# Kernel optimization log

Measured on AMD Instinct MI355X. Metric: run time of the kernel, lower is better.

## Reference

```python
import jax, jax.numpy as jnp
import numpy as np

B, T, C = 4, 2048, 2048
H = 16
DK = C // H // 2          # head_k_dim = 64
DV = C // H               # head_v_dim = 128
KEY_DIM = H * DK          # 1024
VAL_DIM = H * DV          # 2048
CONV = 4                  # short conv kernel size
SCALE = DK ** -0.5


def setup_inputs() -> dict:
    key = jax.random.key(0)
    ks = jax.random.split(key, 12)
    s = 0.02
    rn = lambda k, shape, sc: (jax.random.normal(k, shape) * sc).astype(jnp.float32)
    return dict(
        x=jax.random.normal(ks[0], (B, T, C), jnp.float32),
        qk_w=rn(ks[1], (2 * KEY_DIM, C), s),
        vg_w=rn(ks[2], (2 * VAL_DIM, C), s),
        o_w=rn(ks[3], (C, VAL_DIM), s),
        a_w=rn(ks[4], (H, C), s),
        b_w=rn(ks[5], (H, C), s),
        b_bias=jnp.zeros((H,), jnp.float32),
        beta_bias=jnp.linspace(-1.5, 1.5, H).astype(jnp.float32),
        A_log=jnp.log(jax.random.uniform(ks[6], (H,), minval=2.0, maxval=8.0)).astype(jnp.float32),
        dt_bias=rn(ks[7], (H,), 0.1),
        q_conv_w=rn(ks[8], (KEY_DIM, 1, CONV), 0.3),
        k_conv_w=rn(ks[9], (KEY_DIM, 1, CONV), 0.3),
        v_conv_w=rn(ks[10], (VAL_DIM, 1, CONV), 0.3),
    )


def _causal_dwconv_silu(x, w):
    # x: [B,T,Ch], w: [Ch,1,K]; Conv1d(groups=Ch, padding=K-1) truncated to T == causal conv
    y = jax.lax.conv_general_dilated(
        jnp.transpose(x, (0, 2, 1)), w, (1,), [(w.shape[-1] - 1, 0)],
        dimension_numbers=('NCH', 'OIH', 'NCH'), feature_group_count=x.shape[-1])
    return jax.nn.silu(jnp.transpose(y, (0, 2, 1)))


def _l2norm(x, eps=1e-6):
    return x * jax.lax.rsqrt(jnp.sum(x * x, axis=-1, keepdims=True) + eps)


def _gated_delta_rule(q, k, v, g, beta):
    # q,k: [B,T,H,DK], v: [B,T,H,DV], g,beta: [B,T,H]
    q = _l2norm(q) * SCALE
    k = _l2norm(k)
    # time-major for scan
    qt, kt, vt = (jnp.moveaxis(a, 1, 0) for a in (q, k, v))
    gt, bt = jnp.moveaxis(g, 1, 0), jnp.moveaxis(beta, 1, 0)

    def step(S, inp):
        q_t, k_t, v_t, g_t, b_t = inp          # S: [B,H,DK,DV]
        S = S * jnp.exp(g_t)[..., None, None]  # forget gate
        mem = jnp.einsum('bhk,bhkv->bhv', k_t, S)
        delta = (v_t - mem) * b_t[..., None]   # beta-scaled delta update
        S = S + jnp.einsum('bhk,bhv->bhkv', k_t, delta)
        o_t = jnp.einsum('bhk,bhkv->bhv', q_t, S)
        return S, o_t

    S0 = jnp.zeros((q.shape[0], H, DK, DV), q.dtype)
    _, o = jax.lax.scan(step, S0, (qt, kt, vt, gt, bt))
    return jnp.moveaxis(o, 0, 1)  # [B,T,H,DV]


def reference(x, qk_w, vg_w, o_w, a_w, b_w, b_bias, beta_bias, A_log, dt_bias,
              q_conv_w, k_conv_w, v_conv_w):
    qk = x @ qk_w.T
    vg = x @ vg_w.T
    q, k = qk[..., :KEY_DIM], qk[..., KEY_DIM:]
    v, g_out = vg[..., :VAL_DIM], vg[..., VAL_DIM:]

    q = _causal_dwconv_silu(q, q_conv_w)
    k = _causal_dwconv_silu(k, k_conv_w)
    v = _causal_dwconv_silu(v, v_conv_w)

    Bm, Tm = x.shape[0], x.shape[1]
    q = q.reshape(Bm, Tm, H, DK)
    k = k.reshape(Bm, Tm, H, DK)
    v = v.reshape(Bm, Tm, H, DV)

    beta = jax.nn.sigmoid(x @ b_w.T + b_bias + beta_bias) * 2.0          # [B,T,H]
    g = -jnp.exp(A_log) * jax.nn.softplus(x @ a_w.T + dt_bias)           # [B,T,H]

    o = _gated_delta_rule(q, k, v, g, beta)                              # [B,T,H,DV]

    eps = jnp.finfo(o.dtype).eps
    o = o * jax.lax.rsqrt(jnp.mean(o * o, axis=-1, keepdims=True) + eps)  # rms_norm (no weight)
    o = o * jax.nn.silu(g_out.reshape(Bm, Tm, H, DV))
    return o.reshape(Bm, Tm, VAL_DIM) @ o_w.T
```

## Files before the change

kernel.cpp:

```cpp
#include <hip/hip_runtime.h>
#include <hip/hip_bf16.h>
#include <stdint.h>

#define B_ 4
#define T_ 2048
#define C_ 2048
#define H_ 16
#define DK_ 64
#define DV_ 128
#define BT_ (B_ * T_)

typedef __attribute__((ext_vector_type(8))) __bf16 bf16x8;
typedef __attribute__((ext_vector_type(4))) float f32x4;

__device__ __forceinline__ unsigned short f2bf(float f) {
    union { float f; uint32_t u; } v; v.f = f;
    uint32_t u = v.u;
    uint32_t r = u + 0x7FFFu + ((u >> 16) & 1u);
    return (unsigned short)(r >> 16);
}
__device__ __forceinline__ float bf2f(unsigned short h) {
    union { uint32_t u; float f; } v; v.u = ((uint32_t)h) << 16; return v.f;
}
__device__ __forceinline__ float siluf(float x) { return x / (1.f + expf(-x)); }

__device__ __forceinline__ float dpp_xor1_add(float x) {
    int t = __builtin_amdgcn_update_dpp(0, __float_as_int(x), 0xB1, 0xF, 0xF, true);
    return x + __int_as_float(t);
}
__device__ __forceinline__ float dpp_xor2_add(float x) {
    int t = __builtin_amdgcn_update_dpp(0, __float_as_int(x), 0x4E, 0xF, 0xF, true);
    return x + __int_as_float(t);
}

__device__ __forceinline__ void split_hl(float x, unsigned short& h, unsigned short& l) {
    unsigned short hu = f2bf(x);
    float lo = x - bf2f(hu);
    h = hu;
    l = (unsigned short)(__float_as_uint(lo) >> 16);
}

__global__ void cast_split_k(const float* __restrict__ in,
                             unsigned short* __restrict__ oh, unsigned short* __restrict__ ol, int n4) {
    int i = blockIdx.x * blockDim.x + threadIdx.x;
    if (i >= n4) return;
    float4 v = ((const float4*)in)[i];
    ushort4 h, l;
    split_hl(v.x, h.x, l.x); split_hl(v.y, h.y, l.y);
    split_hl(v.z, h.z, l.z); split_hl(v.w, h.w, l.w);
    ((ushort4*)oh)[i] = h;
    ((ushort4*)ol)[i] = l;
}

__global__ void cast_plain_k(const float* __restrict__ in, unsigned short* __restrict__ out, int n4) {
    int i = blockIdx.x * blockDim.x + threadIdx.x;
    if (i >= n4) return;
    float4 v = ((const float4*)in)[i];
    ushort4 o;
    o.x = f2bf(v.x); o.y = f2bf(v.y); o.z = f2bf(v.z); o.w = f2bf(v.w);
    ((ushort4*)out)[i] = o;
}

__global__ __launch_bounds__(256)
void cast_all_k(const float* __restrict__ x, const float* __restrict__ qk_w,
                const float* __restrict__ vg_w, const float* __restrict__ o_w,
                unsigned short* __restrict__ xh, unsigned short* __restrict__ xl,
                unsigned short* __restrict__ qkw_h, unsigned short* __restrict__ qkw_l,
                unsigned short* __restrict__ vgw_h, unsigned short* __restrict__ vgw_l,
                unsigned short* __restrict__ ow_bf) {
    const int NX = BT_ * C_ / 4;
    const int NW = 2048 * 2048 / 4;
    int i = blockIdx.x * blockDim.x + threadIdx.x;
    const float* src; unsigned short *dh, *dl; int j; bool split;
    if (i < NX)               { j = i;            src = x;                          dh = xh;    dl = xl;    split = true; }
    else if (i < NX + NW)     { j = i - NX;       src = qk_w;                       dh = qkw_h; dl = qkw_l; split = true; }
    else if (i < NX + 2 * NW) { j = i - NX - NW;  src = vg_w;                       dh = vgw_h; dl = vgw_l; split = true; }
    else if (i < NX + 3 * NW) { j = i - NX - 2*NW; src = vg_w + (size_t)2048*2048;  dh = vgw_h + (size_t)2048*2048; dl = nullptr; split = false; }
    else                      { j = i - NX - 3*NW; src = o_w;                       dh = ow_bf; dl = nullptr; split = false; }
    float4 v = ((const float4*)src)[j];
    ushort4 h, l;
    if (split) {
        split_hl(v.x, h.x, l.x); split_hl(v.y, h.y, l.y);
        split_hl(v.z, h.z, l.z); split_hl(v.w, h.w, l.w);
        ((ushort4*)dh)[j] = h;
        ((ushort4*)dl)[j] = l;
    } else {
        h.x = f2bf(v.x); h.y = f2bf(v.y); h.z = f2bf(v.z); h.w = f2bf(v.w);
        ((ushort4*)dh)[j] = h;
    }
}

__device__ __forceinline__ void gld_lds16(const unsigned short* gptr,
                                          unsigned short* lds_base) {
    __builtin_amdgcn_global_load_lds(
        (const __attribute__((address_space(1))) uint32_t*)(uintptr_t)gptr,
        (__attribute__((address_space(3))) uint32_t*)(uint32_t)(uintptr_t)lds_base,
        16, 0, 0);
}

template<bool DO_LO, bool F32OUT>
__global__ __launch_bounds__(256)
void gemm_bf(const unsigned short* __restrict__ Ah, const unsigned short* __restrict__ Al, int lda,
             const unsigned short* __restrict__ Wh, const unsigned short* __restrict__ Wl,
             void* __restrict__ Cout, int M, int N, int K) {
    __shared__ __align__(16) unsigned short sAh[128 * 64];
    __shared__ __align__(16) unsigned short sWh[128 * 64];
    __shared__ __align__(16) unsigned short sAl[DO_LO ? 128 * 64 : 16];
    __shared__ __align__(16) unsigned short sWl[DO_LO ? 128 * 64 : 16];
    const int tid  = threadIdx.x;
    const int wave = tid >> 6;
    const int lane = tid & 63;
    const int wm = (wave >> 1) * 64;
    const int wn = (wave & 1) * 64;
    const int bm = blockIdx.y, bn = blockIdx.x;
    const int srow = lane >> 3;
    const int scol = (lane & 7) * 8;

    const unsigned short* Agh = Ah + (size_t)(bm * 128) * lda;
    const unsigned short* Agl = DO_LO ? (Al + (size_t)(bm * 128) * lda) : nullptr;
    const unsigned short* Wgh = Wh + (size_t)(bn * 128) * K;
    const unsigned short* Wgl = DO_LO ? (Wl + (size_t)(bn * 128) * K) : nullptr;

    f32x4 acc[4][4];
#pragma unroll
    for (int i = 0; i < 4; i++)
#pragma unroll
        for (int j = 0; j < 4; j++) { acc[i][j][0]=0.f; acc[i][j][1]=0.f; acc[i][j][2]=0.f; acc[i][j][3]=0.f; }

    const int mrow = lane & 15;
    const int kq   = (lane >> 4) * 8;

    for (int k0 = 0; k0 < K; k0 += 64) {
#pragma unroll
        for (int i = 0; i < 4; i++) {
            int rbase = wave * 32 + i * 8;
            gld_lds16(Agh + (size_t)(rbase + srow) * lda + k0 + scol, sAh + rbase * 64);
            gld_lds16(Wgh + (size_t)(rbase + srow) * K   + k0 + scol, sWh + rbase * 64);
            if (DO_LO) {
                gld_lds16(Agl + (size_t)(rbase + srow) * lda + k0 + scol, sAl + rbase * 64);
                gld_lds16(Wgl + (size_t)(rbase + srow) * K   + k0 + scol, sWl + rbase * 64);
            }
        }
        __syncthreads();
#pragma unroll
        for (int kk = 0; kk < 2; kk++) {
            bf16x8 afh[4], wfh[4];
#pragma unroll
            for (int i = 0; i < 4; i++)
                afh[i] = *(const bf16x8*)(sAh + (wm + i * 16 + mrow) * 64 + kk * 32 + kq);
#pragma unroll
            for (int j = 0; j < 4; j++)
                wfh[j] = *(const bf16x8*)(sWh + (wn + j * 16 + mrow) * 64 + kk * 32 + kq);
#pragma unroll
            for (int i = 0; i < 4; i++)
#pragma unroll
                for (int j = 0; j < 4; j++)
                    acc[i][j] = __builtin_amdgcn_mfma_f32_16x16x32_bf16(afh[i], wfh[j], acc[i][j], 0, 0, 0);
            if (DO_LO) {
                bf16x8 afl[4], wfl[4];
#pragma unroll
                for (int i = 0; i < 4; i++)
                    afl[i] = *(const bf16x8*)(sAl + (wm + i * 16 + mrow) * 64 + kk * 32 + kq);
#pragma unroll
                for (int j = 0; j < 4; j++)
                    wfl[j] = *(const bf16x8*)(sWl + (wn + j * 16 + mrow) * 64 + kk * 32 + kq);
#pragma unroll
                for (int i = 0; i < 4; i++)
#pragma unroll
                    for (int j = 0; j < 4; j++) {
                        acc[i][j] = __builtin_amdgcn_mfma_f32_16x16x32_bf16(afh[i], wfl[j], acc[i][j], 0, 0, 0);
                        acc[i][j] = __builtin_amdgcn_mfma_f32_16x16x32_bf16(afl[i], wfh[j], acc[i][j], 0, 0, 0);
                    }
            }
        }
        __syncthreads();
    }
    const int r0 = (lane >> 4) * 4;
    const int cn = lane & 15;
#pragma unroll
    for (int i = 0; i < 4; i++) {
#pragma unroll
        for (int r = 0; r < 4; r++) {
            int row = bm * 128 + wm + i * 16 + r0 + r;
            size_t base = (size_t)row * N + bn * 128 + wn + cn;
            if constexpr (F32OUT) {
                float* Crow = (float*)Cout + base;
#pragma unroll
                for (int j = 0; j < 4; j++) Crow[j * 16] = acc[i][j][r];
            } else {
                unsigned short* Crow = (unsigned short*)Cout + base;
#pragma unroll
                for (int j = 0; j < 4; j++) Crow[j * 16] = f2bf(acc[i][j][r]);
            }
        }
    }
}

__global__ __launch_bounds__(256)
void gemm_dual(const unsigned short* __restrict__ Ah, const unsigned short* __restrict__ Al,
               const unsigned short* __restrict__ Wh0, const unsigned short* __restrict__ Wl0, float* __restrict__ C0,
               const unsigned short* __restrict__ Wh1, const unsigned short* __restrict__ Wl1, float* __restrict__ C1) {
    __shared__ __align__(16) unsigned short sAh[128 * 64];
    __shared__ __align__(16) unsigned short sWh[128 * 64];
    __shared__ __align__(16) unsigned short sAl[128 * 64];
    __shared__ __align__(16) unsigned short sWl[128 * 64];
    const int K = 2048, N = 2048, lda = 2048;
    const int tid  = threadIdx.x;
    const int wave = tid >> 6;
    const int lane = tid & 63;
    const int wm = (wave >> 1) * 64;
    const int wn = (wave & 1) * 64;
    const int bm = blockIdx.y;
    const int bnx = blockIdx.x;
    const unsigned short* Wh = (bnx < 16) ? Wh0 : Wh1;
    const unsigned short* Wl = (bnx < 16) ? Wl0 : Wl1;
    float* Csel              = (bnx < 16) ? C0  : C1;
    const int bn = bnx & 15;
    const int srow = lane >> 3;
    const int scol = (lane & 7) * 8;

    const unsigned short* Agh = Ah + (size_t)(bm * 128) * lda;
    const unsigned short* Agl = Al + (size_t)(bm * 128) * lda;
    const unsigned short* Wgh = Wh + (size_t)(bn * 128) * K;
    const unsigned short* Wgl = Wl + (size_t)(bn * 128) * K;

    f32x4 acc[4][4];
#pragma unroll
    for (int i = 0; i < 4; i++)
#pragma unroll
        for (int j = 0; j < 4; j++) { acc[i][j][0]=0.f; acc[i][j][1]=0.f; acc[i][j][2]=0.f; acc[i][j][3]=0.f; }

    const int mrow = lane & 15;
    const int kq   = (lane >> 4) * 8;

    for (int k0 = 0; k0 < K; k0 += 64) {
#pragma unroll
        for (int i = 0; i < 4; i++) {
            int rbase = wave * 32 + i * 8;
            gld_lds16(Agh + (size_t)(rbase + srow) * lda + k0 + scol, sAh + rbase * 64);
            gld_lds16(Wgh + (size_t)(rbase + srow) * K   + k0 + scol, sWh + rbase * 64);
            gld_lds16(Agl + (size_t)(rbase + srow) * lda + k0 + scol, sAl + rbase * 64);
            gld_lds16(Wgl + (size_t)(rbase + srow) * K   + k0 + scol, sWl + rbase * 64);
        }
        __syncthreads();
#pragma unroll
        for (int kk = 0; kk < 2; kk++) {
            bf16x8 afh[4], wfh[4];
#pragma unroll
            for (int i = 0; i < 4; i++)
                afh[i] = *(const bf16x8*)(sAh + (wm + i * 16 + mrow) * 64 + kk * 32 + kq);
#pragma unroll
            for (int j = 0; j < 4; j++)
                wfh[j] = *(const bf16x8*)(sWh + (wn + j * 16 + mrow) * 64 + kk * 32 + kq);
#pragma unroll
            for (int i = 0; i < 4; i++)
#pragma unroll
                for (int j = 0; j < 4; j++)
                    acc[i][j] = __builtin_amdgcn_mfma_f32_16x16x32_bf16(afh[i], wfh[j], acc[i][j], 0, 0, 0);
            bf16x8 afl[4], wfl[4];
#pragma unroll
            for (int i = 0; i < 4; i++)
                afl[i] = *(const bf16x8*)(sAl + (wm + i * 16 + mrow) * 64 + kk * 32 + kq);
#pragma unroll
            for (int j = 0; j < 4; j++)
                wfl[j] = *(const bf16x8*)(sWl + (wn + j * 16 + mrow) * 64 + kk * 32 + kq);
#pragma unroll
            for (int i = 0; i < 4; i++)
#pragma unroll
                for (int j = 0; j < 4; j++) {
                    acc[i][j] = __builtin_amdgcn_mfma_f32_16x16x32_bf16(afh[i], wfl[j], acc[i][j], 0, 0, 0);
                    acc[i][j] = __builtin_amdgcn_mfma_f32_16x16x32_bf16(afl[i], wfh[j], acc[i][j], 0, 0, 0);
                }
        }
        __syncthreads();
    }
    const int r0 = (lane >> 4) * 4;
    const int cn = lane & 15;
#pragma unroll
    for (int i = 0; i < 4; i++) {
#pragma unroll
        for (int r = 0; r < 4; r++) {
            int row = bm * 128 + wm + i * 16 + r0 + r;
            float* Crow = Csel + (size_t)row * N + bn * 128 + wn + cn;
#pragma unroll
            for (int j = 0; j < 4; j++) Crow[j * 16] = acc[i][j][r];
        }
    }
}

template<bool DO_LO, bool F32OUT, bool A_F32>
__global__ __launch_bounds__(512, 2)
void gemm_pc(const void* __restrict__ Aptr, int lda,
             const unsigned short* __restrict__ Wh, const unsigned short* __restrict__ Wl,
             void* __restrict__ Cout, int M, int N, int K) {
    __shared__ __align__(16) unsigned short sAh[2][128 * 64];
    __shared__ __align__(16) unsigned short sWh[2][128 * 64];
// ... 45 lines not shown
    const int wave = tid >> 6;
    const int lane = tid & 63;
    const int wm = (wave >> 1) * 64;
    const int wn = (wave & 1) * 64;
    const int mrow = lane & 15;
    const int kq   = (lane >> 4) * 8;

    f32x4 acc[4][4];
#pragma unroll
    for (int i = 0; i < 4; i++)
#pragma unroll
        for (int j = 0; j < 4; j++) { acc[i][j][0]=0.f; acc[i][j][1]=0.f; acc[i][j][2]=0.f; acc[i][j][3]=0.f; }

    if (!is_cons) stage(0, 0);
    __syncthreads();

    for (int ks = 0; ks < NK; ks++) {
        const int p = ks & 1;
        if (is_cons) {
            const unsigned short* pAh = sAh[p];
            const unsigned short* pWh = sWh[p];
            const unsigned short* pAl = sAl[DO_LO ? p : 0];
            const unsigned short* pWl = sWl[DO_LO ? p : 0];
#pragma unroll
            for (int kk = 0; kk < 2; kk++) {
                bf16x8 afh[4], wfh[4];
#pragma unroll
                for (int i = 0; i < 4; i++)
                    afh[i] = *(const bf16x8*)(pAh + (wm + i * 16 + mrow) * 64 + kk * 32 + kq);
#pragma unroll
                for (int j = 0; j < 4; j++)
                    wfh[j] = *(const bf16x8*)(pWh + (wn + j * 16 + mrow) * 64 + kk * 32 + kq);
#pragma unroll
                for (int i = 0; i < 4; i++)
#pragma unroll
                    for (int j = 0; j < 4; j++)
                        acc[i][j] = __builtin_amdgcn_mfma_f32_16x16x32_bf16(afh[i], wfh[j], acc[i][j], 0, 0, 0);
                if (DO_LO) {
                    bf16x8 afl[4], wfl[4];
#pragma unroll
                    for (int i = 0; i < 4; i++)
                        afl[i] = *(const bf16x8*)(pAl + (wm + i * 16 + mrow) * 64 + kk * 32 + kq);
#pragma unroll
                    for (int j = 0; j < 4; j++)
                        wfl[j] = *(const bf16x8*)(pWl + (wn + j * 16 + mrow) * 64 + kk * 32 + kq);
#pragma unroll
                    for (int i = 0; i < 4; i++)
#pragma unroll
                        for (int j = 0; j < 4; j++) {
                            acc[i][j] = __builtin_amdgcn_mfma_f32_16x16x32_bf16(afh[i], wfl[j], acc[i][j], 0, 0, 0);
                            acc[i][j] = __builtin_amdgcn_mfma_f32_16x16x32_bf16(afl[i], wfh[j], acc[i][j], 0, 0, 0);
                        }
                }
            }
        } else if (ks + 1 < NK) {
            stage(p ^ 1, (ks + 1) * 64);
        }
        __syncthreads();
    }

    if (is_cons) {
        const int r0 = (lane >> 4) * 4;
        const int cn = lane & 15;
#pragma unroll
        for (int i = 0; i < 4; i++) {
#pragma unroll
            for (int r = 0; r < 4; r++) {
                int row = bm * 128 + wm + i * 16 + r0 + r;
                size_t base = (size_t)row * N + bn * 128 + wn + cn;
                if constexpr (F32OUT) {
                    float* Crow = (float*)Cout + base;
#pragma unroll
                    for (int j = 0; j < 4; j++) Crow[j * 16] = acc[i][j][r];
                } else {
                    unsigned short* Crow = (unsigned short*)Cout + base;
#pragma unroll
                    for (int j = 0; j < 4; j++) Crow[j * 16] = f2bf(acc[i][j][r]);
                }
            }
        }
    }
}

__device__ __forceinline__ float softplusf(float x) {
    return (x > 20.f) ? x : log1pf(expf(x));
}

__global__ __launch_bounds__(256)
void gates_k(const float* __restrict__ x, const float* __restrict__ a_w, const float* __restrict__ b_w,
             const float* __restrict__ b_bias, const float* __restrict__ beta_bias,
             const float* __restrict__ A_log, const float* __restrict__ dt_bias,
             float* __restrict__ g, float* __restrict__ beta) {
    int bt = blockIdx.x;
    int wave = threadIdx.x >> 6, lane = threadIdx.x & 63;
    const float* xr = x + (size_t)bt * C_;
#pragma unroll
    for (int dd = 0; dd < 8; dd++) {
        int d = wave * 8 + dd;
        int h = d & 15;
        const float* wr = (d < 16 ? a_w : b_w) + (size_t)h * C_;
        float acc = 0.f;
#pragma unroll
        for (int it = 0; it < 8; it++) {
            float4 xv = ((const float4*)xr)[lane + it * 64];
            float4 wv = ((const float4*)wr)[lane + it * 64];
            acc += xv.x * wv.x + xv.y * wv.y + xv.z * wv.z + xv.w * wv.w;
        }
        acc += __shfl_xor(acc, 1);  acc += __shfl_xor(acc, 2);  acc += __shfl_xor(acc, 4);
        acc += __shfl_xor(acc, 8);  acc += __shfl_xor(acc, 16); acc += __shfl_xor(acc, 32);
        if (lane == 0) {
            if (d < 16) {
                g[(size_t)bt * H_ + h] = -expf(A_log[h]) * softplusf(acc + dt_bias[h]);
            } else {
                float s = 1.f / (1.f + expf(-(acc + b_bias[h] + beta_bias[h])));
                beta[(size_t)bt * H_ + h] = 2.f * s;
            }
        }
    }
}

#define CT_ 32
#define NCH_ (T_ / CT_)

#define LOAD_STEP(t2, kf, qf, vt, dec, btt)                                  \
    {                                                                        \
        _Pragma("unroll")                                                    \
        for (int u = 0; u < 4; u++) {                                        \
            float4 k4 = ((const float4*)(skp + (t2) * 68 + dk0))[u];         \
            float4 q4 = ((const float4*)(sqp + (t2) * 68 + dk0))[u];         \
            kf[u*4+0]=k4.x; kf[u*4+1]=k4.y; kf[u*4+2]=k4.z; kf[u*4+3]=k4.w;  \
            qf[u*4+0]=q4.x; qf[u*4+1]=q4.y; qf[u*4+2]=q4.z; qf[u*4+3]=q4.w;  \
        }                                                                    \
        vt  = svp[(t2) * 68 + dvl];                                          \
        dec = sgp_[(t2)];                                                    \
        btt = sbp_[(t2)];                                                    \
    }

#define DO_STEP(t2, kf, qf, vt, dec, btt)                                    \
    {                                                                        \
        float m0=0.f, m1=0.f, m2=0.f, m3=0.f;                                \
        _Pragma("unroll")                                                    \
        for (int u = 0; u < 4; u++) {                                        \
            m0 += kf[u*4+0]*S[u*4+0]; m1 += kf[u*4+1]*S[u*4+1];              \
            m2 += kf[u*4+2]*S[u*4+2]; m3 += kf[u*4+3]*S[u*4+3];              \
        }                                                                    \
        float m = (m0 + m1) + (m2 + m3);                                     \
        m = dpp_xor1_add(m);                                                 \
        m = dpp_xor2_add(m);                                                 \
        _Pragma("unroll")                                                    \
        for (int i = 0; i < 16; i++) S[i] *= dec;                            \
        float delta = (vt - m * dec) * btt;                                  \
        float o0=0.f, o1=0.f, o2=0.f, o3=0.f;                                \
        _Pragma("unroll")                                                    \
        for (int u = 0; u < 4; u++) {                                        \
            S[u*4+0] += kf[u*4+0]*delta; o0 += qf[u*4+0]*S[u*4+0];           \
            S[u*4+1] += kf[u*4+1]*delta; o1 += qf[u*4+1]*S[u*4+1];           \
            S[u*4+2] += kf[u*4+2]*delta; o2 += qf[u*4+2]*S[u*4+2];           \
            S[u*4+3] += kf[u*4+3]*delta; o3 += qf[u*4+3]*S[u*4+3];           \
        }                                                                    \
        float ov = (o0 + o1) + (o2 + o3);                                    \
        ov = dpp_xor1_add(ov);                                               \
        ov = dpp_xor2_add(ov);                                               \
        if (dkq == 0)                                                        \
            vbuf[vbase + (size_t)(tc + (t2)) * 2048 + dvl] = ov;             \
    }

#define CONSUME_GROUP(TB, TE)                                                \
    {                                                                        \
        float kfa[16], qfa[16], kfb[16], qfb[16];                            \
        float vta, deca, btta, vtb, decb, bttb;                              \
        LOAD_STEP(TB, kfa, qfa, vta, deca, btta);                            \
        int t2 = TB;                                                         \
        _Pragma("unroll 1")                                                  \
        for (; t2 + 2 <= (TE); t2 += 2) {                                    \
            LOAD_STEP(t2 + 1, kfb, qfb, vtb, decb, bttb);                    \
            DO_STEP(t2, kfa, qfa, vta, deca, btta);                          \
            if (t2 + 2 < (TE))                                               \
                LOAD_STEP(t2 + 2, kfa, qfa, vta, deca, btta);                \
            DO_STEP(t2 + 1, kfb, qfb, vtb, decb, bttb);                      \
        }                                                                    \
        if (t2 < (TE))                                                       \
            DO_STEP(t2, kfa, qfa, vta, deca, btta);                          \
    }

__global__ __launch_bounds__(512, 4)
void scan_gemm_k(const float* __restrict__ qk, float* __restrict__ vbuf,
                 const float* __restrict__ qcw, const float* __restrict__ kcw, const float* __restrict__ vcw,
                 const float* __restrict__ g, const float* __restrict__ beta,
                 const unsigned short* __restrict__ xh, const unsigned short* __restrict__ gwh,
                 unsigned short* __restrict__ gout) {
    extern __shared__ char smem_raw[];
    const int blk = blockIdx.x;
    const int tid = threadIdx.x;

    if (blk >= 128) {
        const int bid = blk - 128;
        const int bm = bid >> 4;
        const int bn = bid & 15;
        unsigned short* sA = (unsigned short*)smem_raw;
        unsigned short* sB = sA + 128 * 64;
        const bool act = tid < 256;
        const int wave = tid >> 6;
        const int lane = tid & 63;
        const int wm = (wave >> 1) * 64;
        const int wn = (wave & 1) * 64;
        const int srow = lane >> 3;
        const int scol = (lane & 7) * 8;
        const int mrow = lane & 15;
        const int kq   = (lane >> 4) * 8;
        const unsigned short* Ag = xh  + (size_t)(bm * 128) * 2048;
        const unsigned short* Wg = gwh + (size_t)(bn * 128) * 2048;
        f32x4 acc[4][4];
#pragma unroll
        for (int i = 0; i < 4; i++)
#pragma unroll
            for (int j = 0; j < 4; j++) { acc[i][j][0]=0.f; acc[i][j][1]=0.f; acc[i][j][2]=0.f; acc[i][j][3]=0.f; }
        for (int k0 = 0; k0 < 2048; k0 += 64) {
            if (act) {
#pragma unroll
                for (int i = 0; i < 4; i++) {
                    int rbase = wave * 32 + i * 8;
                    gld_lds16(Ag + (size_t)(rbase + srow) * 2048 + k0 + scol, sA + rbase * 64);
                    gld_lds16(Wg + (size_t)(rbase + srow) * 2048 + k0 + scol, sB + rbase * 64);
                }
            }
            __syncthreads();
            if (act) {
#pragma unroll
                for (int kk = 0; kk < 2; kk++) {
                    bf16x8 af[4], bfr[4];
#pragma unroll
                    for (int i = 0; i < 4; i++)
                        af[i] = *(const bf16x8*)(sA + (wm + i * 16 + mrow) * 64 + kk * 32 + kq);
#pragma unroll
                    for (int j = 0; j < 4; j++)
                        bfr[j] = *(const bf16x8*)(sB + (wn + j * 16 + mrow) * 64 + kk * 32 + kq);
#pragma unroll
                    for (int i = 0; i < 4; i++)
#pragma unroll
                        for (int j = 0; j < 4; j++)
                            acc[i][j] = __builtin_amdgcn_mfma_f32_16x16x32_bf16(af[i], bfr[j], acc[i][j], 0, 0, 0);
                }
            }
            __syncthreads();
        }
        if (act) {
            const int r0 = (lane >> 4) * 4;
            const int cn = lane & 15;
#pragma unroll
            for (int i = 0; i < 4; i++) {
#pragma unroll
                for (int r = 0; r < 4; r++) {
                    int row = bm * 128 + wm + i * 16 + r0 + r;
                    unsigned short* Crow = gout + (size_t)row * 2048 + bn * 128 + wn + cn;
#pragma unroll
                    for (int j = 0; j < 4; j++) Crow[j * 16] = f2bf(acc[i][j][r]);
                }
            }
        }
        return;
    }

    const int vh  = blk & 1;
    const int bh  = blk >> 1;
    const int b   = bh >> 4;
    const int h   = bh & 15;

    float* sqb  = (float*)smem_raw;
    float* skb  = sqb + 2 * CT_ * 68;
    float* svb  = skb + 2 * CT_ * 68;
    float* sgb  = svb + 2 * CT_ * 68;
    float* sbb  = sgb + 2 * CT_;
    float* vcar = sbb + 2 * CT_;

    const size_t qbase = (size_t)b * T_ * 2048 + h * 64;
    const size_t kbase = qbase + 1024;
    const size_t vbase = (size_t)b * T_ * 2048 + h * 128 + vh * 64;
    const size_t gbase = (size_t)b * T_ * H_ + h;

    const bool is_cons = (tid < 256);

    const int ptid = tid - 256;
    const int pc   = ptid & 63;
    const int pw   = ptid >> 6;
    const int R0   = pw * 8;
    float wqa[4], wka[4], wva[4];
    if (!is_cons) {
        float4 a4 = *(const float4*)(qcw + (size_t)(h * 64 + pc) * 4);
        float4 b4 = *(const float4*)(kcw + (size_t)(h * 64 + pc) * 4);
        float4 c4 = *(const float4*)(vcw + (size_t)(h * 128 + vh * 64 + pc) * 4);
        wqa[0]=a4.x; wqa[1]=a4.y; wqa[2]=a4.z; wqa[3]=a4.w;
        wka[0]=b4.x; wka[1]=b4.y; wka[2]=b4.z; wka[3]=b4.w;
        wva[0]=c4.x; wva[1]=c4.y; wva[2]=c4.z; wva[3]=c4.w;
    }

    auto stage = [&](int ci) {
        const int rp  = ci & 1;
        const int tcc = ci * CT_;
        float* dq = sqb + rp * (CT_ * 68);
        float* dk = skb + rp * (CT_ * 68);
        float* dv = svb + rp * (CT_ * 68);
        float qin[11], kin[11], vin[11];
#pragma unroll
        for (int j = 0; j < 11; j++) {
            int rr = tcc + R0 - 3 + j;
            bool ok = (rr >= 0);
            qin[j] = ok ? qk[qbase + (size_t)rr * 2048 + pc] : 0.f;
            kin[j] = ok ? qk[kbase + (size_t)rr * 2048 + pc] : 0.f;
        }
        if (pw == 0) {
#pragma unroll
            for (int j = 0; j < 3; j++) vin[j] = vcar[(rp ^ 1) * 192 + j * 64 + pc];
#pragma unroll
            for (int j = 3; j < 11; j++) vin[j] = vbuf[vbase + (size_t)(tcc + j - 3) * 2048 + pc];
        } else {
#pragma unroll
            for (int j = 0; j < 11; j++) vin[j] = vbuf[vbase + (size_t)(tcc + R0 - 3 + j) * 2048 + pc];
        }
        if (pw == 3) {
#pragma unroll
            for (int j = 0; j < 3; j++) vcar[rp * 192 + j * 64 + pc] = vin[8 + j];
        }
#pragma unroll
        for (int it = 0; it < 8; it++) {
            const int r = R0 + it;
            float aq = 0.f, ak = 0.f, av = 0.f;
#pragma unroll
            for (int j = 0; j < 4; j++) {
                aq += wqa[j] * qin[it + j];
                ak += wka[j] * kin[it + j];
                av += wva[j] * vin[it + j];
            }
            dq[r * 68 + pc] = siluf(aq);
            dk[r * 68 + pc] = siluf(ak);
            dv[r * 68 + pc] = siluf(av);
        }
        if (ptid < CT_)          sgb[rp * CT_ + ptid]       = expf(g[gbase + (size_t)(tcc + ptid) * H_]);
        else if (ptid < 2 * CT_) sbb[rp * CT_ + ptid - CT_] = beta[gbase + (size_t)(tcc + ptid - CT_) * H_];
        {
            const int rl = R0 + (pc >> 3);
            const int jc = pc & 7;
            float* kr = dk + rl * 68 + jc * 8;
            float* qr = dq + rl * 68 + jc * 8;
            float4 k0 = ((const float4*)kr)[0], k1 = ((const float4*)kr)[1];
            float4 q0 = ((const float4*)qr)[0], q1 = ((const float4*)qr)[1];
            float ssk = k0.x*k0.x + k0.y*k0.y + k0.z*k0.z + k0.w*k0.w
                      + k1.x*k1.x + k1.y*k1.y + k1.z*k1.z + k1.w*k1.w;
            float ssq = q0.x*q0.x + q0.y*q0.y + q0.z*q0.z + q0.w*q0.w
                      + q1.x*q1.x + q1.y*q1.y + q1.z*q1.z + q1.w*q1.w;
            ssk += __shfl_xor(ssk, 1); ssk += __shfl_xor(ssk, 2); ssk += __shfl_xor(ssk, 4);
            ssq += __shfl_xor(ssq, 1); ssq += __shfl_xor(ssq, 2); ssq += __shfl_xor(ssq, 4);
            float rk_ = rsqrtf(ssk + 1e-6f);
            float rq_ = rsqrtf(ssq + 1e-6f) * 0.125f;
            k0.x*=rk_; k0.y*=rk_; k0.z*=rk_; k0.w*=rk_;
            k1.x*=rk_; k1.y*=rk_; k1.z*=rk_; k1.w*=rk_;
            q0.x*=rq_; q0.y*=rq_; q0.z*=rq_; q0.w*=rq_;
            q1.x*=rq_; q1.y*=rq_; q1.z*=rq_; q1.w*=rq_;
            ((float4*)kr)[0] = k0; ((float4*)kr)[1] = k1;
            ((float4*)qr)[0] = q0; ((float4*)qr)[1] = q1;
        }
    };

    const int dkq = tid & 3;
    const int dvl = tid >> 2;
    const int dk0 = dkq * 16;
    float S[16];
#pragma unroll
    for (int i = 0; i < 16; i++) S[i] = 0.f;

    if (!is_cons) {
        if (pw == 0) {
#pragma unroll
            for (int j = 0; j < 3; j++) vcar[192 + j * 64 + pc] = 0.f;
        }
        stage(0);
    }
    __syncthreads();

    for (int ci = 0; ci < NCH_; ci++) {
        const int p  = ci & 1;
        const int tc = ci * CT_;
        const float* sqp  = sqb + p * (CT_ * 68);
        const float* skp  = skb + p * (CT_ * 68);
        const float* svp  = svb + p * (CT_ * 68);
        const float* sgp_ = sgb + p * CT_;
        const float* sbp_ = sbb + p * CT_;

        if (is_cons) { CONSUME_GROUP(0, CT_); }
        else if (ci + 1 < NCH_) stage(ci + 1);
        __syncthreads();
    }
}

__global__ __launch_bounds__(512)
void scan_fused(const float* __restrict__ qk, float* __restrict__ vbuf,
                const float* __restrict__ qcw, const float* __restrict__ kcw, const float* __restrict__ vcw,
                const float* __restrict__ g, const float* __restrict__ beta) {
    int blk = blockIdx.x;
    int vh  = blk & 1;
    int bh  = blk >> 1;
    int b   = bh >> 4;
    int h   = bh & 15;
    int tid = threadIdx.x;

    __shared__ __align__(16) float rawq[2][(CT_ + 3) * 64];
    __shared__ __align__(16) float rawk[2][(CT_ + 3) * 64];
    __shared__ __align__(16) float rawv[2][(CT_ + 3) * 64];
    __shared__ __align__(16) float sq[2][CT_ * 68];
    __shared__ __align__(16) float sk[2][CT_ * 68];
    __shared__ __align__(16) float sv[2][CT_ * 68];
    __shared__ float sg[2][CT_];
    __shared__ float sb[2][CT_];

    const size_t qbase = (size_t)b * T_ * 2048 + h * 64;
    const size_t kbase = qbase + 1024;
    const size_t vbase = (size_t)b * T_ * 2048 + h * 128 + vh * 64;
    const size_t gbase = (size_t)b * T_ * H_ + h;

    const bool is_cons = (tid < 256);

    const int ptid = tid - 256;
    const int pc   = ptid & 63;
    const int pw   = ptid >> 6;
    float wqa[4], wka[4], wva[4];
    if (!is_cons) {
        float4 a4 = *(const float4*)(qcw + (size_t)(h * 64 + pc) * 4);
        float4 b4 = *(const float4*)(kcw + (size_t)(h * 64 + pc) * 4);
        float4 c4 = *(const float4*)(vcw + (size_t)(h * 128 + vh * 64 + pc) * 4);
        wqa[0]=a4.x; wqa[1]=a4.y; wqa[2]=a4.z; wqa[3]=a4.w;
        wka[0]=b4.x; wka[1]=b4.y; wka[2]=b4.z; wka[3]=b4.w;
        wva[0]=c4.x; wva[1]=c4.y; wva[2]=c4.z; wva[3]=c4.w;
        if (ptid < 192) {
            int bsel = ptid >> 6, c = ptid & 63;
            float* rb = bsel == 0 ? rawq[1] : (bsel == 1 ? rawk[1] : rawv[1]);
#pragma unroll
            for (int j = 0; j < 3; j++) rb[(CT_ + j) * 64 + c] = 0.f;
        }
    }

    auto prod_phase1 = [&](int ci) {
        int rp = ci & 1;
        int tcc = ci * CT_;
        float* rq = rawq[rp]; float* rk = rawk[rp]; float* rv = rawv[rp];
        const float* pq = rawq[rp ^ 1]; const float* pk = rawk[rp ^ 1]; const float* pv = rawv[rp ^ 1];
        if (ptid < 192) {
            int bsel = ptid >> 6, c = ptid & 63;
            float*       db = bsel == 0 ? rq : (bsel == 1 ? rk : rv);
            const float* sc = bsel == 0 ? pq : (bsel == 1 ? pk : pv);
#pragma unroll
            for (int j = 0; j < 3; j++) db[j * 64 + c] = sc[(CT_ + j) * 64 + c];
        }
#pragma unroll
        for (int u = 0; u < 2; u++) {
            int idx = u * 256 + ptid;
            int r   = idx >> 4;
            int c4  = (idx & 15) * 4;
            size_t row = (size_t)(tcc + r) * 2048;
            *(float4*)(rq + (3 + r) * 64 + c4) = *(const float4*)(qk + qbase + row + c4);
            *(float4*)(rk + (3 + r) * 64 + c4) = *(const float4*)(qk + kbase + row + c4);
            *(float4*)(rv + (3 + r) * 64 + c4) = *(const float4*)(vbuf + vbase + row + c4);
        }
        if (ptid < CT_)          sg[rp][ptid]       = expf(g[gbase + (size_t)(tcc + ptid) * H_]);
        else if (ptid < 2 * CT_) sb[rp][ptid - CT_] = beta[gbase + (size_t)(tcc + ptid - CT_) * H_];
    };

    auto prod_phase2 = [&](int ci) {
        int rp = ci & 1;
        const float* rq = rawq[rp]; const float* rk = rawk[rp]; const float* rv = rawv[rp];
        float* dq = sq[rp]; float* dk = sk[rp]; float* dv = sv[rp];
#pragma unroll
        for (int it = 0; it < 8; it++) {
// ... 60 lines not shown

        if (is_cons) { CONSUME_GROUP(0, 11); }
        else if (ci + 1 < NCH_) prod_phase1(ci + 1);
        __syncthreads();
        if (is_cons) { CONSUME_GROUP(11, 22); }
        else if (ci + 1 < NCH_) prod_phase2(ci + 1);
        __syncthreads();
        if (is_cons) { CONSUME_GROUP(22, 32); }
        else if (ci + 1 < NCH_) prod_phase3(ci + 1);
        __syncthreads();
    }
}

__global__ __launch_bounds__(256)
void postnorm_k(float* __restrict__ vbuf, const unsigned short* __restrict__ gout) {
    int bt  = blockIdx.x;
    int tid = threadIdx.x;
    const float* orow = vbuf + (size_t)bt * 2048 + tid * 8;
    float4 a = ((const float4*)orow)[0];
    float4 c = ((const float4*)orow)[1];
    float ss = a.x*a.x + a.y*a.y + a.z*a.z + a.w*a.w
             + c.x*c.x + c.y*c.y + c.z*c.z + c.w*c.w;
    ss += __shfl_xor(ss, 1); ss += __shfl_xor(ss, 2); ss += __shfl_xor(ss, 4); ss += __shfl_xor(ss, 8);
    float rms = rsqrtf(ss * (1.f / 128.f) + 1.1920928955078125e-07f);
    const unsigned short* grow = gout + (size_t)bt * 2048 + tid * 8;
    ushort4 g1 = ((const ushort4*)grow)[0];
    ushort4 g2 = ((const ushort4*)grow)[1];
    ushort4 r0, r1;
    r0.x = f2bf(a.x * rms * siluf(bf2f(g1.x)));
    r0.y = f2bf(a.y * rms * siluf(bf2f(g1.y)));
    r0.z = f2bf(a.z * rms * siluf(bf2f(g1.z)));
    r0.w = f2bf(a.w * rms * siluf(bf2f(g1.w)));
    r1.x = f2bf(c.x * rms * siluf(bf2f(g2.x)));
    r1.y = f2bf(c.y * rms * siluf(bf2f(g2.y)));
    r1.z = f2bf(c.z * rms * siluf(bf2f(g2.z)));
    r1.w = f2bf(c.w * rms * siluf(bf2f(g2.w)));
    __syncthreads();
    unsigned short* og = (unsigned short*)vbuf + (size_t)bt * 4096 + tid * 8;
    *(ushort4*)og       = r0;
    *(ushort4*)(og + 4) = r1;
}

extern "C" void kernel_launch(void* const* d_in, const int* in_sizes, int n_in,
                              void* d_out, int out_size, void* d_ws, size_t ws_size,
                              hipStream_t stream) {
    (void)in_sizes; (void)n_in; (void)out_size;
    const float* x        = (const float*)d_in[0];
    const float* qk_w     = (const float*)d_in[1];
    const float* vg_w     = (const float*)d_in[2];
    const float* o_w      = (const float*)d_in[3];
    const float* a_w      = (const float*)d_in[4];
    const float* b_w      = (const float*)d_in[5];
    const float* b_bias   = (const float*)d_in[6];
    const float* beta_b   = (const float*)d_in[7];
    const float* A_log    = (const float*)d_in[8];
    const float* dt_bias  = (const float*)d_in[9];
    const float* q_conv_w = (const float*)d_in[10];
    const float* k_conv_w = (const float*)d_in[11];
    const float* v_conv_w = (const float*)d_in[12];

    char* ws = (char*)d_ws;
    float* qkf            = (float*)d_out;
    float* outp           = (float*)d_out;

    if (ws_size >= (size_t)177u * 1024u * 1024u) {
        unsigned short* xh    = (unsigned short*)(ws);
        unsigned short* xl    = (unsigned short*)(ws + (32u << 20));
        unsigned short* qkw_h = (unsigned short*)(ws + (64u << 20));
        unsigned short* qkw_l = (unsigned short*)(ws + (72u << 20));
        unsigned short* vgw_h = (unsigned short*)(ws + (80u << 20));
        unsigned short* vgw_l = (unsigned short*)(ws + (96u << 20));
        unsigned short* ow_bf = (unsigned short*)(ws + (104u << 20));
        float*          vbuf  = (float*)(ws + (112u << 20));
        float*          gbuf  = (float*)(ws + (176u << 20));
        float*          bbuf  = (float*)(ws + (176u << 20) + (512u << 10));
        unsigned short* goutb = xl;

        {
            const int NTOT = BT_ * C_ / 4 + 4 * (2048 * 2048 / 4);
            cast_all_k<<<NTOT / 256, 256, 0, stream>>>(x, qk_w, vg_w, o_w,
                xh, xl, qkw_h, qkw_l, vgw_h, vgw_l, ow_bf);
        }

        gemm_dual<<<dim3(32, 64), 256, 0, stream>>>(xh, xl, qkw_h, qkw_l, qkf, vgw_h, vgw_l, vbuf);

        gates_k<<<BT_, 256, 0, stream>>>(x, a_w, b_w, b_bias, beta_b, A_log, dt_bias, gbuf, bbuf);

        scan_gemm_k<<<128 + 1024, 512, 54272, stream>>>(
            qkf, vbuf, q_conv_w, k_conv_w, v_conv_w, gbuf, bbuf,
            xh, vgw_h + (size_t)2048 * 2048, goutb);

        postnorm_k<<<BT_, 256, 0, stream>>>(vbuf, goutb);

        gemm_bf<false, true><<<dim3(16, 64), 256, 0, stream>>>(
            (const unsigned short*)vbuf, nullptr, 4096, ow_bf, nullptr, outp, BT_, 2048, 2048);
    } else {
        unsigned short* qkw_h = (unsigned short*)(ws);
        unsigned short* qkw_l = (unsigned short*)(ws + (8u  << 20));
        unsigned short* vgw_h = (unsigned short*)(ws + (16u << 20));
        unsigned short* vgw_l = (unsigned short*)(ws + (32u << 20));
        unsigned short* ow_bf = (unsigned short*)(ws + (48u << 20));
        float*          vbuf  = (float*)(ws + (56u << 20));
        float*          gbuf  = (float*)(ws + (120u << 20));
        float*          bbuf  = (float*)(ws + (120u << 20) + (512u << 10));
        unsigned short* goutb = (unsigned short*)d_out;

        cast_split_k<<<(2048 * 2048 / 4 + 255) / 256, 256, 0, stream>>>(qk_w, qkw_h, qkw_l, 2048 * 2048 / 4);
        cast_split_k<<<(2048 * 2048 / 4 + 255) / 256, 256, 0, stream>>>(vg_w, vgw_h, vgw_l, 2048 * 2048 / 4);
        cast_plain_k<<<(2048 * 2048 / 4 + 255) / 256, 256, 0, stream>>>(
            vg_w + (size_t)2048 * 2048, vgw_h + (size_t)2048 * 2048, 2048 * 2048 / 4);
        cast_plain_k<<<(2048 * 2048 / 4 + 255) / 256, 256, 0, stream>>>(o_w, ow_bf, 2048 * 2048 / 4);

        gemm_pc<true, true, true><<<dim3(16, 64), 512, 0, stream>>>(x, 2048, qkw_h, qkw_l, qkf, BT_, 2048, 2048);
        gemm_pc<true, true, true><<<dim3(16, 64), 512, 0, stream>>>(x, 2048, vgw_h, vgw_l, vbuf, BT_, 2048, 2048);

        gates_k<<<BT_, 256, 0, stream>>>(x, a_w, b_w, b_bias, beta_b, A_log, dt_bias, gbuf, bbuf);

        scan_fused<<<B_ * H_ * 2, 512, 0, stream>>>(qkf, vbuf, q_conv_w, k_conv_w, v_conv_w, gbuf, bbuf);

        gemm_pc<false, false, true><<<dim3(16, 64), 512, 0, stream>>>(
            x, 2048, vgw_h + (size_t)2048 * 2048, nullptr, goutb, BT_, 2048, 2048);

        postnorm_k<<<BT_, 256, 0, stream>>>(vbuf, goutb);

        gemm_pc<false, true, false><<<dim3(16, 64), 512, 0, stream>>>(
            (const void*)vbuf, 4096, ow_bf, nullptr, outp, BT_, 2048, 2048);
    }
}
```

Baseline: 1.358 ms.

## Split scan over four DV quarters, fuse gates into dual GEMM with swizzle

The gated-delta scan now splits each head's value dimension into four 32-wide quarters instead of two halves, so 256 scan blocks run instead of 128. Each consumer thread keeps 8 state elements and reduces across 8 lanes using DPP, including a row-mirror step. The gate projection kernel is folded into the dual QK/VG GEMM launch as extra blocks, and GEMM tiles are remapped with a block-index swizzle for better cache locality. The wider split adds parallelism for the latency-bound recurrence and drops one launch, but q/k conv and staging are now repeated by four blocks per head instead of two.

```diff
diff --git a/kernel.cpp b/kernel.cpp
--- a/kernel.cpp
+++ b/kernel.cpp
@@ -30,6 +30,10 @@
 }
 __device__ __forceinline__ float dpp_xor2_add(float x) {
     int t = __builtin_amdgcn_update_dpp(0, __float_as_int(x), 0x4E, 0xF, 0xF, true);
+    return x + __int_as_float(t);
+}
+__device__ __forceinline__ float dpp_mir8_add(float x) {
+    int t = __builtin_amdgcn_update_dpp(0, __float_as_int(x), 0x141, 0xF, 0xF, true);
     return x + __int_as_float(t);
 }
 
@@ -196,22 +200,76 @@
     }
 }
 
+__device__ __forceinline__ float softplusf(float x) {
+    return (x > 20.f) ? x : log1pf(expf(x));
+}
+
+__device__ __forceinline__ void gates_body(int bt, int tid,
+             const float* __restrict__ x, const float* __restrict__ a_w, const float* __restrict__ b_w,
+             const float* __restrict__ b_bias, const float* __restrict__ beta_bias,
+             const float* __restrict__ A_log, const float* __restrict__ dt_bias,
+             float* __restrict__ g, float* __restrict__ beta) {
+    int wave = tid >> 6, lane = tid & 63;
+    const float* xr = x + (size_t)bt * C_;
+#pragma unroll
+    for (int dd = 0; dd < 8; dd++) {
+        int d = wave * 8 + dd;
+        int h = d & 15;
+        const float* wr = (d < 16 ? a_w : b_w) + (size_t)h * C_;
+        float acc = 0.f;
+#pragma unroll
+        for (int it = 0; it < 8; it++) {
+            float4 xv = ((const float4*)xr)[lane + it * 64];
+            float4 wv = ((const float4*)wr)[lane + it * 64];
+            acc += xv.x * wv.x + xv.y * wv.y + xv.z * wv.z + xv.w * wv.w;
+        }
+        acc += __shfl_xor(acc, 1);  acc += __shfl_xor(acc, 2);  acc += __shfl_xor(acc, 4);
+        acc += __shfl_xor(acc, 8);  acc += __shfl_xor(acc, 16); acc += __shfl_xor(acc, 32);
+        if (lane == 0) {
+            if (d < 16) {
+                g[(size_t)bt * H_ + h] = -expf(A_log[h]) * softplusf(acc + dt_bias[h]);
+            } else {
+                float s = 1.f / (1.f + expf(-(acc + b_bias[h] + beta_bias[h])));
+                beta[(size_t)bt * H_ + h] = 2.f * s;
+            }
+        }
+    }
+}
+
 __global__ __launch_bounds__(256)
-void gemm_dual(const unsigned short* __restrict__ Ah, const unsigned short* __restrict__ Al,
-               const unsigned short* __restrict__ Wh0, const unsigned short* __restrict__ Wl0, float* __restrict__ C0,
-               const unsigned short* __restrict__ Wh1, const unsigned short* __restrict__ Wl1, float* __restrict__ C1) {
+void gates_k(const float* __restrict__ x, const float* __restrict__ a_w, const float* __restrict__ b_w,
+             const float* __restrict__ b_bias, const float* __restrict__ beta_bias,
+             const float* __restrict__ A_log, const float* __restrict__ dt_bias,
+             float* __restrict__ g, float* __restrict__ beta) {
+    gates_body(blockIdx.x, threadIdx.x, x, a_w, b_w, b_bias, beta_bias, A_log, dt_bias, g, beta);
+}
+
+__global__ __launch_bounds__(256)
+void gemm_dual_gates(const unsigned short* __restrict__ Ah, const unsigned short* __restrict__ Al,
+                     const unsigned short* __restrict__ Wh0, const unsigned short* __restrict__ Wl0, float* __restrict__ C0,
+                     const unsigned short* __restrict__ Wh1, const unsigned short* __restrict__ Wl1, float* __restrict__ C1,
+                     const float* __restrict__ x, const float* __restrict__ a_w, const float* __restrict__ b_w,
+                     const float* __restrict__ b_bias, const float* __restrict__ beta_bias,
+                     const float* __restrict__ A_log, const float* __restrict__ dt_bias,
+                     float* __restrict__ g, float* __restrict__ beta) {
+    const int bid = blockIdx.x;
+    const int tid = threadIdx.x;
+    if (bid >= 2048) {
+        gates_body(bid - 2048, tid, x, a_w, b_w, b_bias, beta_bias, A_log, dt_bias, g, beta);
+        return;
+    }
     __shared__ __align__(16) unsigned short sAh[128 * 64];
     __shared__ __align__(16) unsigned short sWh[128 * 64];
     __shared__ __align__(16) unsigned short sAl[128 * 64];
     __shared__ __align__(16) unsigned short sWl[128 * 64];
+    const int wg  = ((bid & 7) << 8) | (bid >> 3);
+    const int bm  = wg >> 5;
+    const int bnx = wg & 31;
     const int K = 2048, N = 2048, lda = 2048;
-    const int tid  = threadIdx.x;
     const int wave = tid >> 6;
     const int lane = tid & 63;
     const int wm = (wave >> 1) * 64;
     const int wn = (wave & 1) * 64;
-    const int bm = blockIdx.y;
-    const int bnx = blockIdx.x;
     const unsigned short* Wh = (bnx < 16) ? Wh0 : Wh1;
     const unsigned short* Wl = (bnx < 16) ? Wl0 : Wl1;
     float* Csel              = (bnx < 16) ? C0  : C1;
@@ -423,45 +481,66 @@
     }
 }
 
-__device__ __forceinline__ float softplusf(float x) {
-    return (x > 20.f) ? x : log1pf(expf(x));
-}
-
-__global__ __launch_bounds__(256)
-void gates_k(const float* __restrict__ x, const float* __restrict__ a_w, const float* __restrict__ b_w,
-             const float* __restrict__ b_bias, const float* __restrict__ beta_bias,
-             const float* __restrict__ A_log, const float* __restrict__ dt_bias,
-             float* __restrict__ g, float* __restrict__ beta) {
-    int bt = blockIdx.x;
-    int wave = threadIdx.x >> 6, lane = threadIdx.x & 63;
-    const float* xr = x + (size_t)bt * C_;
-#pragma unroll
-    for (int dd = 0; dd < 8; dd++) {
-        int d = wave * 8 + dd;
-        int h = d & 15;
-        const float* wr = (d < 16 ? a_w : b_w) + (size_t)h * C_;
-        float acc = 0.f;
-#pragma unroll
-        for (int it = 0; it < 8; it++) {
-            float4 xv = ((const float4*)xr)[lane + it * 64];
-            float4 wv = ((const float4*)wr)[lane + it * 64];
-            acc += xv.x * wv.x + xv.y * wv.y + xv.z * wv.z + xv.w * wv.w;
-        }
-        acc += __shfl_xor(acc, 1);  acc += __shfl_xor(acc, 2);  acc += __shfl_xor(acc, 4);
-        acc += __shfl_xor(acc, 8);  acc += __shfl_xor(acc, 16); acc += __shfl_xor(acc, 32);
-        if (lane == 0) {
-            if (d < 16) {
-                g[(size_t)bt * H_ + h] = -expf(A_log[h]) * softplusf(acc + dt_bias[h]);
-            } else {
-                float s = 1.f / (1.f + expf(-(acc + b_bias[h] + beta_bias[h])));
-                beta[(size_t)bt * H_ + h] = 2.f * s;
-            }
-        }
-    }
-}
-
 #define CT_ 32
 #define NCH_ (T_ / CT_)
+
+#define LOAD_STEP8(t2, kf, qf, vt, dec, btt)                                 \
+    {                                                                        \
+        float4 ka = ((const float4*)(skp + (t2) * 68 + dk0))[0];             \
+        float4 kb = ((const float4*)(skp + (t2) * 68 + dk0))[1];             \
+        float4 qa = ((const float4*)(sqp + (t2) * 68 + dk0))[0];             \
+        float4 qb = ((const float4*)(sqp + (t2) * 68 + dk0))[1];             \
+        kf[0]=ka.x; kf[1]=ka.y; kf[2]=ka.z; kf[3]=ka.w;                      \
+        kf[4]=kb.x; kf[5]=kb.y; kf[6]=kb.z; kf[7]=kb.w;                      \
+        qf[0]=qa.x; qf[1]=qa.y; qf[2]=qa.z; qf[3]=qa.w;                      \
+        qf[4]=qb.x; qf[5]=qb.y; qf[6]=qb.z; qf[7]=qb.w;                      \
+        vt  = svp[(t2) * 33 + dvl];                                          \
+        dec = sgp_[(t2)];                                                    \
+        btt = sbp_[(t2)];                                                    \
+    }
+
+#define DO_STEP8(t2, kf, qf, vt, dec, btt)                                   \
+    {                                                                        \
+        float m0 = kf[0]*S[0]; float m1 = kf[1]*S[1];                        \
+        float m2 = kf[2]*S[2]; float m3 = kf[3]*S[3];                        \
+        m0 += kf[4]*S[4]; m1 += kf[5]*S[5];                                  \
+        m2 += kf[6]*S[6]; m3 += kf[7]*S[7];                                  \
+        float m = (m0 + m1) + (m2 + m3);                                     \
+        m = dpp_xor1_add(m); m = dpp_xor2_add(m); m = dpp_mir8_add(m);       \
+        _Pragma("unroll")                                                    \
+        for (int i = 0; i < 8; i++) S[i] *= dec;                             \
+        float delta = (vt - m * dec) * btt;                                  \
+        S[0] += kf[0]*delta; float o0 = qf[0]*S[0];                          \
+        S[1] += kf[1]*delta; float o1 = qf[1]*S[1];                          \
+        S[2] += kf[2]*delta; float o2 = qf[2]*S[2];                          \
+        S[3] += kf[3]*delta; float o3 = qf[3]*S[3];                          \
+        S[4] += kf[4]*delta; o0 += qf[4]*S[4];                               \
+        S[5] += kf[5]*delta; o1 += qf[5]*S[5];                               \
+        S[6] += kf[6]*delta; o2 += qf[6]*S[6];                               \
+        S[7] += kf[7]*delta; o3 += qf[7]*S[7];                               \
+        float ov = (o0 + o1) + (o2 + o3);                                    \
+        ov = dpp_xor1_add(ov); ov = dpp_xor2_add(ov); ov = dpp_mir8_add(ov); \
+        if (dkq == 0)                                                        \
+            vbuf[vbase + (size_t)(tc + (t2)) * 2048 + dvl] = ov;             \
+    }
+
+#define CONSUME_GROUP8(TB, TE)                                               \
+    {                                                                        \
+        float kfa[8], qfa[8], kfb[8], qfb[8];                                \
+        float vta, deca, btta, vtb, decb, bttb;                              \
+        LOAD_STEP8(TB, kfa, qfa, vta, deca, btta);                           \
+        int t2 = TB;                                                         \
+        _Pragma("unroll 1")                                                  \
+        for (; t2 + 2 <= (TE); t2 += 2) {                                    \
+            LOAD_STEP8(t2 + 1, kfb, qfb, vtb, decb, bttb);                   \
+            DO_STEP8(t2, kfa, qfa, vta, deca, btta);                         \
+            if (t2 + 2 < (TE))                                               \
+                LOAD_STEP8(t2 + 2, kfa, qfa, vta, deca, btta);               \
+            DO_STEP8(t2 + 1, kfb, qfb, vtb, decb, bttb);                     \
+        }                                                                    \
+        if (t2 < (TE))                                                       \
+            DO_STEP8(t2, kfa, qfa, vta, deca, btta);                         \
+    }
 
 #define LOAD_STEP(t2, kf, qf, vt, dec, btt)                                  \
     {                                                                        \
@@ -534,8 +613,8 @@
     const int blk = blockIdx.x;
     const int tid = threadIdx.x;
 
-    if (blk >= 128) {
-        const int bid = blk - 128;
+    if (blk >= 256) {
+        const int bid = blk - 256;
         const int bm = bid >> 4;
         const int bn = bid & 15;
         unsigned short* sA = (unsigned short*)smem_raw;
@@ -602,21 +681,21 @@
         return;
     }
 
-    const int vh  = blk & 1;
-    const int bh  = blk >> 1;
+    const int vq  = blk & 3;
+    const int bh  = blk >> 2;
     const int b   = bh >> 4;
     const int h   = bh & 15;
 
     float* sqb  = (float*)smem_raw;
     float* skb  = sqb + 2 * CT_ * 68;
     float* svb  = skb + 2 * CT_ * 68;
-    float* sgb  = svb + 2 * CT_ * 68;
+    float* sgb  = svb + 2 * CT_ * 33;
     float* sbb  = sgb + 2 * CT_;
     float* vcar = sbb + 2 * CT_;
 
     const size_t qbase = (size_t)b * T_ * 2048 + h * 64;
     const size_t kbase = qbase + 1024;
-    const size_t vbase = (size_t)b * T_ * 2048 + h * 128 + vh * 64;
+    const size_t vbase = (size_t)b * T_ * 2048 + h * 128 + vq * 32;
     const size_t gbase = (size_t)b * T_ * H_ + h;
 
     const bool is_cons = (tid < 256);
@@ -629,10 +708,12 @@
     if (!is_cons) {
         float4 a4 = *(const float4*)(qcw + (size_t)(h * 64 + pc) * 4);
         float4 b4 = *(const float4*)(kcw + (size_t)(h * 64 + pc) * 4);
-        float4 c4 = *(const float4*)(vcw + (size_t)(h * 128 + vh * 64 + pc) * 4);
         wqa[0]=a4.x; wqa[1]=a4.y; wqa[2]=a4.z; wqa[3]=a4.w;
         wka[0]=b4.x; wka[1]=b4.y; wka[2]=b4.z; wka[3]=b4.w;
-        wva[0]=c4.x; wva[1]=c4.y; wva[2]=c4.z; wva[3]=c4.w;
+        if (pc < 32) {
+            float4 c4 = *(const float4*)(vcw + (size_t)(h * 128 + vq * 32 + pc) * 4);
+            wva[0]=c4.x; wva[1]=c4.y; wva[2]=c4.z; wva[3]=c4.w;
+        }
     }
 
     auto stage = [&](int ci) {
@@ -640,7 +721,7 @@
         const int tcc = ci * CT_;
         float* dq = sqb + rp * (CT_ * 68);
         float* dk = skb + rp * (CT_ * 68);
-        float* dv = svb + rp * (CT_ * 68);
+        float* dv = svb + rp * (CT_ * 33);
         float qin[11], kin[11], vin[11];
 #pragma unroll
         for (int j = 0; j < 11; j++) {
@@ -649,32 +730,38 @@
             qin[j] = ok ? qk[qbase + (size_t)rr * 2048 + pc] : 0.f;
             kin[j] = ok ? qk[kbase + (size_t)rr * 2048 + pc] : 0.f;
         }
-        if (pw == 0) {
-#pragma unroll
-            for (int j = 0; j < 3; j++) vin[j] = vcar[(rp ^ 1) * 192 + j * 64 + pc];
-#pragma unroll
-            for (int j = 3; j < 11; j++) vin[j] = vbuf[vbase + (size_t)(tcc + j - 3) * 2048 + pc];
-        } else {
-#pragma unroll
-            for (int j = 0; j < 11; j++) vin[j] = vbuf[vbase + (size_t)(tcc + R0 - 3 + j) * 2048 + pc];
-        }
-        if (pw == 3) {
-#pragma unroll
-            for (int j = 0; j < 3; j++) vcar[rp * 192 + j * 64 + pc] = vin[8 + j];
+        if (pc < 32) {
+            if (pw == 0) {
+#pragma unroll
+                for (int j = 0; j < 3; j++) vin[j] = vcar[(rp ^ 1) * 96 + j * 32 + pc];
+#pragma unroll
+                for (int j = 3; j < 11; j++) vin[j] = vbuf[vbase + (size_t)(tcc + j - 3) * 2048 + pc];
+            } else {
+#pragma unroll
+                for (int j = 0; j < 11; j++) vin[j] = vbuf[vbase + (size_t)(tcc + R0 - 3 + j) * 2048 + pc];
+            }
+            if (pw == 3) {
+#pragma unroll
+                for (int j = 0; j < 3; j++) vcar[rp * 96 + j * 32 + pc] = vin[8 + j];
+            }
         }
 #pragma unroll
         for (int it = 0; it < 8; it++) {
             const int r = R0 + it;
-            float aq = 0.f, ak = 0.f, av = 0.f;
+            float aq = 0.f, ak = 0.f;
 #pragma unroll
             for (int j = 0; j < 4; j++) {
                 aq += wqa[j] * qin[it + j];
                 ak += wka[j] * kin[it + j];
-                av += wva[j] * vin[it + j];
             }
             dq[r * 68 + pc] = siluf(aq);
             dk[r * 68 + pc] = siluf(ak);
-            dv[r * 68 + pc] = siluf(av);
+            if (pc < 32) {
+                float av = 0.f;
+#pragma unroll
+                for (int j = 0; j < 4; j++) av += wva[j] * vin[it + j];
+                dv[r * 33 + pc] = siluf(av);
+            }
         }
         if (ptid < CT_)          sgb[rp * CT_ + ptid]       = expf(g[gbase + (size_t)(tcc + ptid) * H_]);
         else if (ptid < 2 * CT_) sbb[rp * CT_ + ptid - CT_] = beta[gbase + (size_t)(tcc + ptid - CT_) * H_];
@@ -702,17 +789,17 @@
         }
     };
 
-    const int dkq = tid & 3;
-    const int dvl = tid >> 2;
-    const int dk0 = dkq * 16;
-    float S[16];
-#pragma unroll
-    for (int i = 0; i < 16; i++) S[i] = 0.f;
+    const int dkq = tid & 7;
+    const int dvl = (tid >> 3) & 31;
+    const int dk0 = dkq * 8;
+    float S[8];
+#pragma unroll
+    for (int i = 0; i < 8; i++) S[i] = 0.f;
 
     if (!is_cons) {
-        if (pw == 0) {
-#pragma unroll
-            for (int j = 0; j < 3; j++) vcar[192 + j * 64 + pc] = 0.f;
+        if (pw == 0 && pc < 32) {
+#pragma unroll
+            for (int j = 0; j < 3; j++) vcar[96 + j * 32 + pc] = 0.f;
         }
         stage(0);
     }
@@ -723,11 +810,11 @@
         const int tc = ci * CT_;
         const float* sqp  = sqb + p * (CT_ * 68);
         const float* skp  = skb + p * (CT_ * 68);
-        const float* svp  = svb + p * (CT_ * 68);
+        const float* svp  = svb + p * (CT_ * 33);
         const float* sgp_ = sgb + p * CT_;
         const float* sbp_ = sbb + p * CT_;
 
-        if (is_cons) { CONSUME_GROUP(0, CT_); }
+        if (is_cons) { CONSUME_GROUP8(0, CT_); }
         else if (ci + 1 < NCH_) stage(ci + 1);
         __syncthreads();
     }
@@ -954,13 +1041,16 @@
                 xh, xl, qkw_h, qkw_l, vgw_h, vgw_l, ow_bf);
         }
 
-        gemm_dual<<<dim3(32, 64), 256, 0, stream>>>(xh, xl, qkw_h, qkw_l, qkf, vgw_h, vgw_l, vbuf);
-
-        gates_k<<<BT_, 256, 0, stream>>>(x, a_w, b_w, b_bias, beta_b, A_log, dt_bias, gbuf, bbuf);
-
-        scan_gemm_k<<<128 + 1024, 512, 54272, stream>>>(
-            qkf, vbuf, q_conv_w, k_conv_w, v_conv_w, gbuf, bbuf,
-            xh, vgw_h + (size_t)2048 * 2048, goutb);
+        gemm_dual_gates<<<2048 + BT_, 256, 0, stream>>>(
+            xh, xl, qkw_h, qkw_l, qkf, vgw_h, vgw_l, vbuf,
+            x, a_w, b_w, b_bias, beta_b, A_log, dt_bias, gbuf, bbuf);
+
+        {
+            const int scan_lds = (2*CT_*68 + 2*CT_*68 + 2*CT_*33 + 2*CT_ + 2*CT_ + 2*3*32) * 4;
+            scan_gemm_k<<<256 + 1024, 512, scan_lds, stream>>>(
+                qkf, vbuf, q_conv_w, k_conv_w, v_conv_w, gbuf, bbuf,
+                xh, vgw_h + (size_t)2048 * 2048, goutb);
+        }
 
         postnorm_k<<<BT_, 256, 0, stream>>>(vbuf, goutb);
 
```

Result: faster. 1.273 ms (-6.3%).
